# Performance work log

Measured on AMD Instinct MI355X. Metric: run time of the kernel, lower is better.

## Reference

```python
import jax, jax.numpy as jnp
import numpy as np

N = 50000      # num atoms
E = 800000     # num edges
F = 64         # atom_fea_len
NBR = 64       # nbr_fea_len
NCONV = 3
T = 4096       # pooled target atoms
STATE = 2
VOCAB = 100
EPS = 1e-5


def setup_inputs() -> dict:
    key = jax.random.key(0)
    ks = jax.random.split(key, 20)
    Z = 2 * F + NBR  # concat message width
    inp = {
        "x_types": jax.random.randint(ks[0], (N,), 0, VOCAB),
        "edge_index": jax.random.randint(ks[1], (2, E), 0, N),
        "edge_attr": jax.random.normal(ks[2], (E, NBR), dtype=jnp.float32),
        "target": jax.random.randint(ks[3], (T,), 0, N),
        "emb": jax.random.normal(ks[4], (VOCAB, F), dtype=jnp.float32),
        "Wc": jax.random.normal(ks[5], (NCONV, F, Z), dtype=jnp.float32) * 0.05,
        "bc": jnp.zeros((NCONV, F), jnp.float32),
        "Wf": jax.random.normal(ks[6], (NCONV, 1, Z), dtype=jnp.float32) * 0.05,
        "bf": jnp.zeros((NCONV, 1), jnp.float32),
        "g1": jnp.ones((NCONV, F), jnp.float32),
        "b1": jnp.zeros((NCONV, F), jnp.float32),
        "g2": jnp.ones((NCONV, F), jnp.float32),
        "b2": jnp.zeros((NCONV, F), jnp.float32),
        "Wfc": jax.random.normal(ks[7], (F, F), dtype=jnp.float32) * 0.05,
        "bfc": jnp.zeros((F,), jnp.float32),
        "Ws": jax.random.normal(ks[8], (STATE, F), dtype=jnp.float32) * 0.05,
        "bs": jnp.zeros((STATE,), jnp.float32),
    }
    return inp


def _segment_softmax(logits, idx, n):
    # per-target-node softmax over variable-size edge neighborhoods
    m = jax.ops.segment_max(logits, idx, num_segments=n)
    m = jnp.where(jnp.isfinite(m), m, 0.0)
    e = jnp.exp(logits - m[idx])
    s = jax.ops.segment_sum(e, idx, num_segments=n)
    return e / (s[idx] + 1e-16)


def _batchnorm(x, gamma, beta):
    # training-mode BatchNorm1d: biased batch stats over dim 0
    mu = x.mean(0)
    var = x.var(0)
    return (x - mu) * jax.lax.rsqrt(var + EPS) * gamma + beta


def reference(x_types, edge_index, edge_attr, target, emb, Wc, bc, Wf, bf,
              g1, b1, g2, b2, Wfc, bfc, Ws, bs):
    x = emb[x_types]                      # [N, F]
    # flow='target_to_source': i = edge_index[0] (aggregate here), j = edge_index[1]
    idx_i = edge_index[0]
    idx_j = edge_index[1]
    ones = jnp.ones((edge_index.shape[1],), x.dtype)
    cnt = jax.ops.segment_sum(ones, idx_i, num_segments=x.shape[0])
    denom = jnp.maximum(cnt, 1.0)[:, None]
    for l in range(NCONV):
        z = jnp.concatenate([x[idx_i], x[idx_j], edge_attr], axis=1)  # [E, 2F+NBR]
        core = jax.nn.relu(_batchnorm(z @ Wc[l].T + bc[l], g1[l], b1[l]))  # [E, F]
        filt = (z @ Wf[l].T + bf[l])[:, 0]                                  # [E]
        alpha = _segment_softmax(filt, idx_i, x.shape[0])[:, None]          # [E, 1]
        agg = jax.ops.segment_sum(alpha * core, idx_i, num_segments=x.shape[0]) / denom
        x = jax.nn.relu(_batchnorm(agg, g2[l], b2[l]) + x)
    h = jax.nn.relu(x[target])            # [T, F]
    h = jax.nn.relu(h @ Wfc.T + bfc)
    logits = h @ Ws.T + bs                # [T, STATE]
    return jax.nn.softmax(logits, axis=-1)
```

## Files before the change

kernel.cpp:

```cpp
#include <hip/hip_runtime.h>
#include <math.h>

#define N_ATOMS 50000
#define N_EDGES 800000
#define F 64
#define Z 192
#define NCONV 3
#define T_TGT 4096
#define EPS 1e-5f
#define SLOTS 64
#define NB_SCAN 196
#define TILE_E 128
#define TPB_TILES 5
#define NBLK_MM 1250

typedef __attribute__((ext_vector_type(4))) float f32x4;
typedef __attribute__((ext_vector_type(8))) short s16x8;
typedef __attribute__((ext_vector_type(8))) __bf16 bf16x8;

static_assert(NBLK_MM * TPB_TILES * TILE_E == N_EDGES, "tiling exact");

static __device__ __forceinline__ float bf2f(unsigned short u) {
    return __uint_as_float(((unsigned int)u) << 16);
}
static __device__ __forceinline__ unsigned short f2bf(float f) {
    unsigned int u = __float_as_uint(f);
    unsigned int r = u + 0x7FFFu + ((u >> 16) & 1u);
    return (unsigned short)(r >> 16);
}
static __device__ __forceinline__ bf16x8 pack8(float4 a, float4 b) {
    s16x8 r;
    r[0] = (short)f2bf(a.x); r[1] = (short)f2bf(a.y);
    r[2] = (short)f2bf(a.z); r[3] = (short)f2bf(a.w);
    r[4] = (short)f2bf(b.x); r[5] = (short)f2bf(b.y);
    r[6] = (short)f2bf(b.z); r[7] = (short)f2bf(b.w);
    return __builtin_bit_cast(bf16x8, r);
}


__global__ void k_embed(const int* __restrict__ types, const float* __restrict__ emb,
                        float* __restrict__ x, unsigned short* __restrict__ xb) {
    int idx = blockIdx.x * 256 + threadIdx.x;
    if (idx < N_ATOMS * F) {
        int n = idx >> 6, f = idx & 63;
        float v = emb[types[n] * F + f];
        x[idx] = v;
        xb[idx] = f2bf(v);
    }
}

__global__ void k_degree(const int* __restrict__ idx_i, int* __restrict__ cnt) {
    int e = blockIdx.x * 256 + threadIdx.x;
    if (e < N_EDGES) atomicAdd(&cnt[idx_i[e]], 1);
}

__global__ void k_scanA(const int* __restrict__ cnt, int* __restrict__ bsum) {
    __shared__ int s[256];
    int base = blockIdx.x * 256, t = threadIdx.x;
    s[t] = (base + t < N_ATOMS) ? cnt[base + t] : 0;
    __syncthreads();
    for (int o = 128; o > 0; o >>= 1) {
        if (t < o) s[t] += s[t + o];
        __syncthreads();
    }
    if (t == 0) bsum[blockIdx.x] = s[0];
}

__global__ void k_scanB(int* __restrict__ bsum, int* __restrict__ rowptr) {
    __shared__ int s[256];
    int t = threadIdx.x;
    int v = (t < NB_SCAN) ? bsum[t] : 0;
    s[t] = v;
    __syncthreads();
    for (int o = 1; o < 256; o <<= 1) {
        int add = (t >= o) ? s[t - o] : 0;
        __syncthreads();
        s[t] += add;
        __syncthreads();
    }
    if (t < NB_SCAN) bsum[t] = s[t] - v;
    if (t == 0) rowptr[N_ATOMS] = N_EDGES;
}

__global__ void k_scanC(const int* __restrict__ cnt, const int* __restrict__ bsum,
                        int* __restrict__ rowptr) {
    __shared__ int s[256];
    int base = blockIdx.x * 256, t = threadIdx.x;
    int v = (base + t < N_ATOMS) ? cnt[base + t] : 0;
    s[t] = v;
    __syncthreads();
    for (int o = 1; o < 256; o <<= 1) {
        int add = (t >= o) ? s[t - o] : 0;
        __syncthreads();
        s[t] += add;
        __syncthreads();
    }
    if (base + t < N_ATOMS) rowptr[base + t] = bsum[blockIdx.x] + s[t] - v;
}

__global__ void k_scatter(const int* __restrict__ idx_i, const int* __restrict__ idx_j,
                          const int* __restrict__ rowptr, int* __restrict__ wofs,
                          int* __restrict__ i_s, int* __restrict__ j_s,
                          int* __restrict__ eperm) {
    int e = blockIdx.x * 256 + threadIdx.x;
    if (e < N_EDGES) {
        int i = idx_i[e];
        int pos = rowptr[i] + atomicAdd(&wofs[i], 1);
        i_s[pos] = i;
        j_s[pos] = idx_j[e];
        eperm[pos] = e;
    }
}

__global__ void k_ea_cvt(const float* __restrict__ ea, const int* __restrict__ eperm,
                         unsigned short* __restrict__ eab) {
    int idx = blockIdx.x * 256 + threadIdx.x;
    int row = idx >> 3;
    int seg = (idx & 7) * 8;
    if (row < N_EDGES) {
        const float* src = ea + (size_t)eperm[row] * F + seg;
        float4 a = *(const float4*)src;
        float4 b = *(const float4*)(src + 4);
        bf16x8 r = pack8(a, b);
        *(bf16x8*)(eab + (size_t)row * F + seg) = r;
    }
}

__global__ __launch_bounds__(256, 2) void k_edge_mfma(
    const unsigned short* __restrict__ xb, const unsigned short* __restrict__ eab,
    const int* __restrict__ i_s, const int* __restrict__ j_s,
    const float* __restrict__ Wc, const float* __restrict__ Wf,
    unsigned short* __restrict__ y, float* __restrict__ filt,
    float* __restrict__ stats)
{
    int t = threadIdx.x;
    int lane = t & 63, w = t >> 6;
    int c = lane & 15, g = lane >> 4;
    int goff = g * 8;

    bf16x8 Bf[6][5];
    #pragma unroll
    for (int nt = 0; nt < 4; ++nt) {
        const float* wrow = Wc + (size_t)(nt * 16 + c) * Z;
        #pragma unroll
        for (int kt = 0; kt < 6; ++kt) {
            const float* wp = wrow + kt * 32 + goff;
            float4 w0 = *(const float4*)wp;
            float4 w1 = *(const float4*)(wp + 4);
            Bf[kt][nt] = pack8(w0, w1);
        }
    }
    #pragma unroll
    for (int kt = 0; kt < 6; ++kt) {
        s16x8 zz = {0, 0, 0, 0, 0, 0, 0, 0};
        bf16x8 r = __builtin_bit_cast(bf16x8, zz);
        if (c == 0) {
            const float* wp = Wf + kt * 32 + goff;
            float4 w0 = *(const float4*)wp;
            float4 w1 = *(const float4*)(wp + 4);
            r = pack8(w0, w1);
        }
        Bf[kt][4] = r;
    }

    int tile = blockIdx.x * TPB_TILES;

    bf16x8 Af[2][6];
    #pragma unroll
    for (int m = 0; m < 2; ++m) {
        int e = tile * TILE_E + (w * 2 + m) * 16 + c;
        const unsigned short* bi = xb + (size_t)i_s[e] * F + goff;
        const unsigned short* bj = xb + (size_t)j_s[e] * F + goff;
        const unsigned short* be = eab + (size_t)e * F + goff;
        Af[m][0] = *(const bf16x8*)(bi);
        Af[m][1] = *(const bf16x8*)(bi + 32);
        Af[m][2] = *(const bf16x8*)(bj);
        Af[m][3] = *(const bf16x8*)(bj + 32);
        Af[m][4] = *(const bf16x8*)(be);
        Af[m][5] = *(const bf16x8*)(be + 32);
    }

    float ssum[4] = {0.f, 0.f, 0.f, 0.f};
    float ssq[4]  = {0.f, 0.f, 0.f, 0.f};

    for (int it = 0; it < TPB_TILES; ++it) {
        int cur = tile + it;
        int nxt = (it + 1 < TPB_TILES) ? cur + 1 : cur;
        const unsigned short *bi2[2], *bj2[2], *be2[2];
        #pragma unroll
        for (int m = 0; m < 2; ++m) {
            int e = nxt * TILE_E + (w * 2 + m) * 16 + c;
            bi2[m] = xb + (size_t)i_s[e] * F + goff;
            bj2[m] = xb + (size_t)j_s[e] * F + goff;
            be2[m] = eab + (size_t)e * F + goff;
        }

        f32x4 acc[2][5];
        #pragma unroll
        for (int m = 0; m < 2; ++m)
            #pragma unroll
            for (int nt = 0; nt < 5; ++nt)
                acc[m][nt] = (f32x4){0.f, 0.f, 0.f, 0.f};

        #pragma unroll
        for (int kt = 0; kt < 6; ++kt) {
            #pragma unroll
            for (int m = 0; m < 2; ++m) {
                #pragma unroll
                for (int nt = 0; nt < 5; ++nt)
                    acc[m][nt] = __builtin_amdgcn_mfma_f32_16x16x32_bf16(
                        Af[m][kt], Bf[kt][nt], acc[m][nt], 0, 0, 0);
            }
            #pragma unroll
            for (int m = 0; m < 2; ++m) {
                const unsigned short* p = (kt < 2) ? bi2[m] : (kt < 4) ? bj2[m] : be2[m];
                Af[m][kt] = *(const bf16x8*)(p + (kt & 1) * 32);
            }
        }

        #pragma unroll
        for (int m = 0; m < 2; ++m) {
            int ebase = cur * TILE_E + (w * 2 + m) * 16 + g * 4;
            #pragma unroll
            for (int nt = 0; nt < 4; ++nt) {
                #pragma unroll
                for (int q = 0; q < 4; ++q) {
                    float v = acc[m][nt][q];
                    y[(size_t)(ebase + q) * F + nt * 16 + c] = f2bf(v);
                    ssum[nt] += v;
                    ssq[nt] += v * v;
                }
            }
            if (c == 0) {
                #pragma unroll
                for (int q = 0; q < 4; ++q) filt[ebase + q] = acc[m][4][q];
            }
        }
    }

    int slot = (blockIdx.x & (SLOTS - 1)) * 128;
    #pragma unroll
    for (int nt = 0; nt < 4; ++nt) {
        float S = ssum[nt], Q = ssq[nt];
        S += __shfl_xor(S, 16, 64); S += __shfl_xor(S, 32, 64);
        Q += __shfl_xor(Q, 16, 64); Q += __shfl_xor(Q, 32, 64);
        if (g == 0) {
            atomicAdd(&stats[slot + nt * 16 + c], S);
            atomicAdd(&stats[slot + 64 + nt * 16 + c], Q);
        }
    }
}


__global__ void k_finbn(const float* __restrict__ stats, float* __restrict__ bnp, float count) {
    int f = threadIdx.x;
    float S = 0.f, Q = 0.f;
    for (int s = 0; s < SLOTS; ++s) {
        S += stats[s * 128 + f];
        Q += stats[s * 128 + 64 + f];
    }
    float mu = S / count;
    float var = Q / count - mu * mu;
    var = fmaxf(var, 0.f);
    bnp[f] = mu;
    bnp[64 + f] = 1.f / sqrtf(var + EPS);
}

__global__ __launch_bounds__(256) void k_node_agg(
    const unsigned short* __restrict__ y, const float* __restrict__ filt,
    const int* __restrict__ rowptr, const int* __restrict__ cnt,
    const float* __restrict__ bnp, const float* __restrict__ g1, const float* __restrict__ b1,
    float* __restrict__ agg)
{
    int t = threadIdx.x;
    int lane = t & 63;
    int node = blockIdx.x * 4 + (t >> 6);
    if (node >= N_ATOMS) return;
    int beg = rowptr[node], end = rowptr[node + 1];
    float mu = bnp[lane], rstd = bnp[64 + lane];
    float ga = g1[lane], be = b1[lane];
    float fm = -INFINITY;
    for (int i = beg + lane; i < end; i += 64) fm = fmaxf(fm, filt[i]);
    #pragma unroll
    for (int o = 32; o > 0; o >>= 1) fm = fmaxf(fm, __shfl_xor(fm, o, 64));
    float acc = 0.f, ssum = 0.f;
    for (int e = beg; e < end; ++e) {
        float wgt = expf(filt[e] - fm);
        float yv = bf2f(y[(size_t)e * F + lane]);
        float core = fmaxf((yv - mu) * rstd * ga + be, 0.f);
        acc += wgt * core;
        ssum += wgt;
    }
    float dn = fmaxf((float)cnt[node], 1.f);
    agg[(size_t)node * F + lane] = acc / (ssum + 1e-16f) / dn;
}

__global__ void k_colstats(const float* __restrict__ agg, float* __restrict__ stats) {
    __shared__ float buf[4][64];
    int t = threadIdx.x;
    int f = t & 63, g = t >> 6;
    float S = 0.f, Q = 0.f;
    for (int n = blockIdx.x * 4 + g; n < N_ATOMS; n += gridDim.x * 4) {
        float v = agg[(size_t)n * F + f];
        S += v; Q += v * v;
    }
    buf[g][f] = S;
    __syncthreads();
    if (t < 64) {
        float s2 = buf[0][t] + buf[1][t] + buf[2][t] + buf[3][t];
        atomicAdd(&stats[(blockIdx.x & 63) * 128 + t], s2);
    }
    __syncthreads();
    buf[g][f] = Q;
    __syncthreads();
    if (t < 64) {
        float q2 = buf[0][t] + buf[1][t] + buf[2][t] + buf[3][t];
        atomicAdd(&stats[(blockIdx.x & 63) * 128 + 64 + t], q2);
    }
}

__global__ void k_node_upd(const float* __restrict__ agg, const float* __restrict__ bnp,
                           const float* __restrict__ g2, const float* __restrict__ b2,
                           const float* __restrict__ xin, float* __restrict__ xout,
                           unsigned short* __restrict__ xbout) {
    int idx = blockIdx.x * 256 + threadIdx.x;
    if (idx < N_ATOMS * F) {
        int f = idx & 63;
        float v = (agg[idx] - bnp[f]) * bnp[64 + f] * g2[f] + b2[f] + xin[idx];
        v = fmaxf(v, 0.f);
        xout[idx] = v;
        xbout[idx] = f2bf(v);
    }
}


__global__ __launch_bounds__(256) void k_head(
    const float* __restrict__ x, const int* __restrict__ target,
    const float* __restrict__ Wfc, const float* __restrict__ bfc,
    const float* __restrict__ Ws, const float* __restrict__ bs,
    float* __restrict__ out)
{
    __shared__ float hbuf[4][64];
    int t = threadIdx.x;
    int lane = t & 63, w = t >> 6;
    int tt = blockIdx.x * 4 + w;
    int a = target[min(tt, T_TGT - 1)];
    float h = fmaxf(x[(size_t)a * F + lane], 0.f);
    hbuf[w][lane] = h;
    __syncthreads();
    float acc = bfc[lane];
    #pragma unroll 8
    for (int k = 0; k < F; ++k) acc += hbuf[w][k] * Wfc[lane * F + k];
    float h2 = fmaxf(acc, 0.f);
    float p0 = h2 * Ws[lane];
    float p1 = h2 * Ws[F + lane];
    #pragma unroll
    for (int o = 32; o > 0; o >>= 1) {
        p0 += __shfl_xor(p0, o, 64);
        p1 += __shfl_xor(p1, o, 64);
    }
    if (lane == 0 && tt < T_TGT) {
        float l0 = p0 + bs[0], l1 = p1 + bs[1];
        float mx = fmaxf(l0, l1);
        float e0v = expf(l0 - mx), e1v = expf(l1 - mx);
        float inv = 1.f / (e0v + e1v);
        out[tt * 2 + 0] = e0v * inv;
        out[tt * 2 + 1] = e1v * inv;
    }
}


extern "C" void kernel_launch(void* const* d_in, const int* in_sizes, int n_in,
                              void* d_out, int out_size, void* d_ws, size_t ws_size,
                              hipStream_t stream)
{
    const int*   x_types = (const int*)d_in[0];
    const int*   eidx    = (const int*)d_in[1];
    const float* ea      = (const float*)d_in[2];
    const int*   target  = (const int*)d_in[3];
    const float* emb     = (const float*)d_in[4];
    const float* Wc      = (const float*)d_in[5];
    const float* Wf      = (const float*)d_in[7];
    const float* g1      = (const float*)d_in[9];
    const float* b1      = (const float*)d_in[10];
    const float* g2      = (const float*)d_in[11];
    const float* b2      = (const float*)d_in[12];
    const float* Wfc     = (const float*)d_in[13];
    const float* bfc     = (const float*)d_in[14];
    const float* Ws      = (const float*)d_in[15];
    const float* bs      = (const float*)d_in[16];
    float* out = (float*)d_out;
    const int* idx_i = eidx;
    const int* idx_j = eidx + N_EDGES;

    char* p = (char*)d_ws;
    auto alloc = [&](size_t bytes) {
        char* r = p;
        p += (bytes + 255) & ~(size_t)255;
        return r;
    };
    float* xa            = (float*)alloc((size_t)N_ATOMS * F * 4);
    float* xb_f          = (float*)alloc((size_t)N_ATOMS * F * 4);
    unsigned short* x16a = (unsigned short*)alloc((size_t)N_ATOMS * F * 2);
    unsigned short* x16b = (unsigned short*)alloc((size_t)N_ATOMS * F * 2);
    unsigned short* eab  = (unsigned short*)alloc((size_t)N_EDGES * F * 2);
    unsigned short* ybuf = (unsigned short*)alloc((size_t)N_EDGES * F * 2);
    float* filt          = (float*)alloc((size_t)N_EDGES * 4);
    float* agg           = (float*)alloc((size_t)N_ATOMS * F * 4);
    int* cnt             = (int*)alloc((size_t)N_ATOMS * 4);
    int* rowptr          = (int*)alloc((size_t)(N_ATOMS + 1) * 4);
    int* wofs            = (int*)alloc((size_t)N_ATOMS * 4);
    int* i_s             = (int*)alloc((size_t)N_EDGES * 4);
    int* j_s             = (int*)alloc((size_t)N_EDGES * 4);
    int* eperm           = (int*)alloc((size_t)N_EDGES * 4);
    int* bsum            = (int*)alloc(256 * 4);
    float* stats         = (float*)alloc(SLOTS * 128 * 4);
    float* bnp1          = (float*)alloc(128 * 4);
    float* bnp2          = (float*)alloc(128 * 4);
    (void)ws_size; (void)in_sizes; (void)n_in; (void)out_size;

    hipMemsetAsync(cnt, 0, (size_t)N_ATOMS * 4, stream);
    hipMemsetAsync(wofs, 0, (size_t)N_ATOMS * 4, stream);
    k_embed<<<(N_ATOMS * F + 255) / 256, 256, 0, stream>>>(x_types, emb, xa, x16a);
    k_degree<<<(N_EDGES + 255) / 256, 256, 0, stream>>>(idx_i, cnt);
    k_scanA<<<NB_SCAN, 256, 0, stream>>>(cnt, bsum);
    k_scanB<<<1, 256, 0, stream>>>(bsum, rowptr);
    k_scanC<<<NB_SCAN, 256, 0, stream>>>(cnt, bsum, rowptr);
    k_scatter<<<(N_EDGES + 255) / 256, 256, 0, stream>>>(idx_i, idx_j, rowptr, wofs,
                                                         i_s, j_s, eperm);
    k_ea_cvt<<<(N_EDGES * 8 + 255) / 256, 256, 0, stream>>>(ea, eperm, eab);

    float* xcur = xa;
    float* xnxt = xb_f;
    unsigned short* x16cur = x16a;
    unsigned short* x16nxt = x16b;
    for (int l = 0; l < NCONV; ++l) {
        hipMemsetAsync(stats, 0, SLOTS * 128 * 4, stream);
        k_edge_mfma<<<NBLK_MM, 256, 0, stream>>>(
            x16cur, eab, i_s, j_s,
            Wc + (size_t)l * F * Z, Wf + (size_t)l * Z,
            ybuf, filt, stats);
        k_finbn<<<1, 64, 0, stream>>>(stats, bnp1, (float)N_EDGES);
        k_node_agg<<<N_ATOMS / 4, 256, 0, stream>>>(ybuf, filt, rowptr, cnt, bnp1,
                                                    g1 + (size_t)l * F, b1 + (size_t)l * F, agg);
        hipMemsetAsync(stats, 0, SLOTS * 128 * 4, stream);
        k_colstats<<<256, 256, 0, stream>>>(agg, stats);
        k_finbn<<<1, 64, 0, stream>>>(stats, bnp2, (float)N_ATOMS);
        k_node_upd<<<(N_ATOMS * F + 255) / 256, 256, 0, stream>>>(
            agg, bnp2, g2 + (size_t)l * F, b2 + (size_t)l * F, xcur, xnxt, x16nxt);
        float* tf = xcur; xcur = xnxt; xnxt = tf;
        unsigned short* ts = x16cur; x16cur = x16nxt; x16nxt = ts;
    }
    k_head<<<T_TGT / 4, 256, 0, stream>>>(xcur, target, Wfc, bfc, Ws, bs, out);
}
```

Before: 858.9 us.

## Stage edge weights in LDS for occupancy and vectorize node aggregation over edges

Moves the bf16 weight fragments for the edge MFMA kernel from per-thread registers into shared memory and raises the launch bound to three blocks per SM, to reduce register pressure and improve latency hiding. Rewrites node aggregation so each wavefront processes four edges per iteration with 4-wide feature loads and a cross-lane shuffle reduction, increasing memory-level parallelism. This adds LDS reads per k-step in the MFMA loop, and the aggregation removes its bounds check, relying on an exact grid.

```diff
diff --git a/kernel.cpp b/kernel.cpp
--- a/kernel.cpp
+++ b/kernel.cpp
@@ -126,42 +126,41 @@
     }
 }
 
-__global__ __launch_bounds__(256, 2) void k_edge_mfma(
+__global__ __launch_bounds__(256, 3) void k_edge_mfma(
     const unsigned short* __restrict__ xb, const unsigned short* __restrict__ eab,
     const int* __restrict__ i_s, const int* __restrict__ j_s,
     const float* __restrict__ Wc, const float* __restrict__ Wf,
     unsigned short* __restrict__ y, float* __restrict__ filt,
     float* __restrict__ stats)
 {
+    __shared__ unsigned short BfL[30 * 64 * 8];
+
     int t = threadIdx.x;
     int lane = t & 63, w = t >> 6;
     int c = lane & 15, g = lane >> 4;
     int goff = g * 8;
 
-    bf16x8 Bf[6][5];
-    #pragma unroll
-    for (int nt = 0; nt < 4; ++nt) {
-        const float* wrow = Wc + (size_t)(nt * 16 + c) * Z;
-        #pragma unroll
-        for (int kt = 0; kt < 6; ++kt) {
-            const float* wp = wrow + kt * 32 + goff;
-            float4 w0 = *(const float4*)wp;
-            float4 w1 = *(const float4*)(wp + 4);
-            Bf[kt][nt] = pack8(w0, w1);
+    #pragma unroll
+    for (int rep = 0; rep < 8; ++rep) {
+        int f = rep * 4 + w;
+        if (f < 30) {
+            int kt = f / 5, nt = f - kt * 5;
+            bf16x8 val;
+            if (nt < 4) {
+                const float* wp = Wc + (size_t)(nt * 16 + c) * Z + kt * 32 + goff;
+                val = pack8(*(const float4*)wp, *(const float4*)(wp + 4));
+            } else {
+                s16x8 zz = {0, 0, 0, 0, 0, 0, 0, 0};
+                val = __builtin_bit_cast(bf16x8, zz);
+                if (c == 0) {
+                    const float* wp = Wf + kt * 32 + goff;
+                    val = pack8(*(const float4*)wp, *(const float4*)(wp + 4));
+                }
+            }
+            *(bf16x8*)(BfL + ((size_t)f * 64 + lane) * 8) = val;
         }
     }
-    #pragma unroll
-    for (int kt = 0; kt < 6; ++kt) {
-        s16x8 zz = {0, 0, 0, 0, 0, 0, 0, 0};
-        bf16x8 r = __builtin_bit_cast(bf16x8, zz);
-        if (c == 0) {
-            const float* wp = Wf + kt * 32 + goff;
-            float4 w0 = *(const float4*)wp;
-            float4 w1 = *(const float4*)(wp + 4);
-            r = pack8(w0, w1);
-        }
-        Bf[kt][4] = r;
-    }
+    __syncthreads();
 
     int tile = blockIdx.x * TPB_TILES;
 
@@ -204,12 +203,19 @@
 
         #pragma unroll
         for (int kt = 0; kt < 6; ++kt) {
+            const unsigned short* bb = BfL + ((size_t)(kt * 5) * 64 + lane) * 8;
+            bf16x8 b0 = *(const bf16x8*)(bb);
+            bf16x8 b1 = *(const bf16x8*)(bb + 512);
+            bf16x8 b2 = *(const bf16x8*)(bb + 1024);
+            bf16x8 b3 = *(const bf16x8*)(bb + 1536);
+            bf16x8 b4 = *(const bf16x8*)(bb + 2048);
             #pragma unroll
             for (int m = 0; m < 2; ++m) {
-                #pragma unroll
-                for (int nt = 0; nt < 5; ++nt)
-                    acc[m][nt] = __builtin_amdgcn_mfma_f32_16x16x32_bf16(
-                        Af[m][kt], Bf[kt][nt], acc[m][nt], 0, 0, 0);
+                acc[m][0] = __builtin_amdgcn_mfma_f32_16x16x32_bf16(Af[m][kt], b0, acc[m][0], 0, 0, 0);
+                acc[m][1] = __builtin_amdgcn_mfma_f32_16x16x32_bf16(Af[m][kt], b1, acc[m][1], 0, 0, 0);
+                acc[m][2] = __builtin_amdgcn_mfma_f32_16x16x32_bf16(Af[m][kt], b2, acc[m][2], 0, 0, 0);
+                acc[m][3] = __builtin_amdgcn_mfma_f32_16x16x32_bf16(Af[m][kt], b3, acc[m][3], 0, 0, 0);
+                acc[m][4] = __builtin_amdgcn_mfma_f32_16x16x32_bf16(Af[m][kt], b4, acc[m][4], 0, 0, 0);
             }
             #pragma unroll
             for (int m = 0; m < 2; ++m) {
@@ -275,24 +281,46 @@
     int t = threadIdx.x;
     int lane = t & 63;
     int node = blockIdx.x * 4 + (t >> 6);
-    if (node >= N_ATOMS) return;
     int beg = rowptr[node], end = rowptr[node + 1];
-    float mu = bnp[lane], rstd = bnp[64 + lane];
-    float ga = g1[lane], be = b1[lane];
+    int es = lane >> 4, fq = lane & 15;
+    float4 mu4 = *(const float4*)(bnp + fq * 4);
+    float4 rs4 = *(const float4*)(bnp + 64 + fq * 4);
+    float4 ga4 = *(const float4*)(g1 + fq * 4);
+    float4 be4 = *(const float4*)(b1 + fq * 4);
+
     float fm = -INFINITY;
     for (int i = beg + lane; i < end; i += 64) fm = fmaxf(fm, filt[i]);
     #pragma unroll
     for (int o = 32; o > 0; o >>= 1) fm = fmaxf(fm, __shfl_xor(fm, o, 64));
-    float acc = 0.f, ssum = 0.f;
-    for (int e = beg; e < end; ++e) {
-        float wgt = expf(filt[e] - fm);
-        float yv = bf2f(y[(size_t)e * F + lane]);
-        float core = fmaxf((yv - mu) * rstd * ga + be, 0.f);
-        acc += wgt * core;
-        ssum += wgt;
-    }
-    float dn = fmaxf((float)cnt[node], 1.f);
-    agg[(size_t)node * F + lane] = acc / (ssum + 1e-16f) / dn;
+
+    float a0 = 0.f, a1 = 0.f, a2 = 0.f, a3 = 0.f, ss = 0.f;
+    for (int base = beg; base < end; base += 4) {
+        int ee = base + es;
+        int eec = min(ee, end - 1);
+        float wgt = (ee < end) ? expf(filt[eec] - fm) : 0.f;
+        ushort4 yv = *(const ushort4*)(y + (size_t)eec * F + fq * 4);
+        float c0 = fmaxf((bf2f(yv.x) - mu4.x) * rs4.x * ga4.x + be4.x, 0.f);
+        float c1 = fmaxf((bf2f(yv.y) - mu4.y) * rs4.y * ga4.y + be4.y, 0.f);
+        float c2 = fmaxf((bf2f(yv.z) - mu4.z) * rs4.z * ga4.z + be4.z, 0.f);
+        float c3 = fmaxf((bf2f(yv.w) - mu4.w) * rs4.w * ga4.w + be4.w, 0.f);
+        a0 += wgt * c0; a1 += wgt * c1; a2 += wgt * c2; a3 += wgt * c3;
+        ss += wgt;
+    }
+    #pragma unroll
+    for (int o = 16; o <= 32; o <<= 1) {
+        a0 += __shfl_xor(a0, o, 64);
+        a1 += __shfl_xor(a1, o, 64);
+        a2 += __shfl_xor(a2, o, 64);
+        a3 += __shfl_xor(a3, o, 64);
+        ss += __shfl_xor(ss, o, 64);
+    }
+    if (lane < 16) {
+        float dn = fmaxf((float)cnt[node], 1.f);
+        float inv = 1.f / ((ss + 1e-16f) * dn);
+        float4 o4;
+        o4.x = a0 * inv; o4.y = a1 * inv; o4.z = a2 * inv; o4.w = a3 * inv;
+        *(float4*)(agg + (size_t)node * F + fq * 4) = o4;
+    }
 }
 
 __global__ void k_colstats(const float* __restrict__ agg, float* __restrict__ stats) {
```

After: 891.1 us. 1.04x slower.
